# Kernel tuning notes

Hardware: AMD Instinct MI355X
Metric: run time of the kernel (lower is better)

## Reference

```python
import jax, jax.numpy as jnp
import numpy as np

B, N, D, H, COND = 1, 1024, 1024, 16, 128
S = 2 * N          # noisy tokens + clean x0 tokens
BS = 16            # diffusion block size
HD = D // H        # head dim = 64


def _ln(x, w):
    # LayerNorm module: F.layer_norm in fp32, then scale by weight (no bias)
    x = x.astype(jnp.float32)
    mu = jnp.mean(x, axis=-1, keepdims=True)
    var = jnp.var(x, axis=-1, keepdims=True)
    return (x - mu) / jnp.sqrt(var + 1e-5) * w


def _rotate_half(x):
    x1, x2 = jnp.split(x, 2, axis=-1)
    return jnp.concatenate([-x2, x1], axis=-1)


def _block_diff_mask(s, n, bs):
    q = jnp.arange(s)[:, None]
    k = jnp.arange(s)[None, :]
    fq = q >= n
    fk = k >= n
    bq = jnp.where(fq, (q - n) // bs, q // bs)
    bk = jnp.where(fk, (k - n) // bs, k // bs)
    diag = (bq == bk) & (fq == fk)
    off = (bq > bk) & fk & (~fq)
    caus = (bq >= bk) & fk & fq
    return diag | off | caus


def setup_inputs() -> dict:
    key = jax.random.key(0)
    ks = jax.random.split(key, 8)
    inv = 1.0 / (10000.0 ** (jnp.arange(0, HD, 2, dtype=jnp.float32) / HD))  # [32]
    t = jnp.arange(N, dtype=jnp.float32)[:, None] * inv[None, :]
    return {
        "x": jax.random.normal(ks[0], (B, S, D), jnp.float32),
        "c": jax.random.normal(ks[1], (B, COND), jnp.float32),
        "cos": jnp.cos(t),
        "sin": jnp.sin(t),
        "norm1_w": jnp.ones((D,), jnp.float32),
        "qkv_w": jax.random.normal(ks[2], (3 * D, D), jnp.float32) * (D ** -0.5),
        "attn_out_w": jax.random.normal(ks[3], (D, D), jnp.float32) * (D ** -0.5),
        "norm2_w": jnp.ones((D,), jnp.float32),
        "mlp_w1": jax.random.normal(ks[4], (4 * D, D), jnp.float32) * (D ** -0.5),
        "mlp_b1": jnp.zeros((4 * D,), jnp.float32),
        "mlp_w2": jax.random.normal(ks[5], (D, 4 * D), jnp.float32) * ((4 * D) ** -0.5),
        "mlp_b2": jnp.zeros((D,), jnp.float32),
        "adaLN_w": jax.random.normal(ks[6], (6 * D, COND), jnp.float32) * 0.02,
        "adaLN_b": jax.random.normal(ks[7], (6 * D,), jnp.float32) * 0.02,
    }


def reference(x, c, cos, sin, norm1_w, qkv_w, attn_out_w, norm2_w,
              mlp_w1, mlp_b1, mlp_w2, mlp_b2, adaLN_w, adaLN_b):
    # adaLN modulation: [B, 6D] -> six [B, 1, D] tensors
    mods = (c @ adaLN_w.T + adaLN_b)[:, None, :]
    sh_msa, sc_msa, g_msa, sh_mlp, sc_mlp, g_mlp = jnp.split(mods, 6, axis=-1)

    x_skip = x
    h = _ln(x, norm1_w) * (1 + sc_msa) + sh_msa  # modulate_fused

    # rotary tables broadcast to qkv rank 5 (torchscript path: applied to q, k AND v)
    cs = jnp.concatenate([cos, cos], axis=-1)[None, :, None, None, :]  # [1,N,1,1,HD]
    sn = jnp.concatenate([sin, sin], axis=-1)[None, :, None, None, :]

    def qkv_of(xh):  # xh: [B, N, D]
        qkv = (xh @ qkv_w.T).reshape(B, N, 3, H, HD)
        return qkv * cs + _rotate_half(qkv) * sn

    # halves processed separately (both use positions 0..N-1), then concatenated
    qkv = jnp.concatenate([qkv_of(h[:, :N]), qkv_of(h[:, N:])], axis=1)  # [B,S,3,H,HD]

    q = jnp.transpose(qkv[:, :, 0], (0, 2, 1, 3))  # [B,H,S,HD]
    k = jnp.transpose(qkv[:, :, 1], (0, 2, 1, 3))
    v = jnp.transpose(qkv[:, :, 2], (0, 2, 1, 3))

    scores = jnp.einsum('bhqd,bhkd->bhqk', q, k) / np.sqrt(HD).astype(np.float32)
    mask = _block_diff_mask(S, N, BS)  # [S,S] bool, block-diag | offset-causal | block-causal
    scores = jnp.where(mask[None, None], scores, -jnp.inf)
    attn = jax.nn.softmax(scores, axis=-1)
    o = jnp.einsum('bhqk,bhkd->bhqd', attn, v)
    o = jnp.transpose(o, (0, 2, 1, 3)).reshape(B, S, D)

    # inference bias_dropout_add_scale: gate * out + residual (dropout is identity)
    x2 = g_msa * (o @ attn_out_w.T) + x_skip
    h2 = _ln(x2, norm2_w) * (1 + sc_mlp) + sh_mlp
    m = jax.nn.gelu(h2 @ mlp_w1.T + mlp_b1, approximate=True) @ mlp_w2.T + mlp_b2
    return g_mlp * m + x2
```

## Files before the change

### kernel.cpp

```cpp
#include <hip/hip_runtime.h>
#include <math.h>

#define SS 2048
#define NN 1024
#define DD 1024
#define HH 16
#define CONDD 128

typedef unsigned short ushort;
typedef unsigned int uint;
typedef __bf16 bf16x8 __attribute__((ext_vector_type(8)));
typedef float f32x4 __attribute__((ext_vector_type(4)));
typedef short s16x4 __attribute__((ext_vector_type(4)));
typedef ushort u16x8 __attribute__((ext_vector_type(8)));

__device__ __forceinline__ float gelu_fast(float x) {
    float t = x + 0.044715f * x * x * x;
    float e = __builtin_exp2f(-2.3022081446f * t);
    return x * __builtin_amdgcn_rcpf(1.0f + e);
}

__device__ __forceinline__ ushort f2bf(float x) {
    uint u = __float_as_uint(x);
    u += 0x7fff + ((u >> 16) & 1);
    return (ushort)(u >> 16);
}

__device__ __forceinline__ float bf2f(ushort u) {
    return __uint_as_float(((uint)u) << 16);
}

__device__ __forceinline__ void gload16(const ushort* g, ushort* l) {
    __builtin_amdgcn_global_load_lds(
        (const __attribute__((address_space(1))) void*)g,
        (__attribute__((address_space(3))) void*)l, 16, 0, 0);
}

__device__ __forceinline__ f32x4 mfma16(s16x4 a, s16x4 b, f32x4 c) {
#if __has_builtin(__builtin_amdgcn_mfma_f32_16x16x16bf16_1k)
    return __builtin_amdgcn_mfma_f32_16x16x16bf16_1k(a, b, c, 0, 0, 0);
#else
    asm("v_mfma_f32_16x16x16_bf16 %0, %1, %2, %0" : "+v"(c) : "v"(a), "v"(b));
    return c;
#endif
}

__global__ void k_cast4(const float* __restrict__ s0, const float* __restrict__ s1,
                        const float* __restrict__ s2, const float* __restrict__ s3,
                        ushort* __restrict__ dst) {
    size_t gid = ((size_t)blockIdx.x * 256 + threadIdx.x) * 4;
    const float* src;
    size_t off;
    if (gid < (3ull << 20))      { src = s0; off = 0; }
    else if (gid < (4ull << 20)) { src = s1; off = 3ull << 20; }
    else if (gid < (8ull << 20)) { src = s2; off = 4ull << 20; }
    else                         { src = s3; off = 8ull << 20; }
    float4 v = *(const float4*)(src + (gid - off));
    ushort4 o = {f2bf(v.x), f2bf(v.y), f2bf(v.z), f2bf(v.w)};
    *(ushort4*)(dst + gid) = o;
}

__global__ void k_adaln(const float* __restrict__ c, const float* __restrict__ w,
                        const float* __restrict__ b, float* __restrict__ mods) {
    int o = blockIdx.x * 256 + threadIdx.x;
    float s = b[o];
    const float* wr = w + (size_t)o * CONDD;
    for (int k = 0; k < CONDD; ++k) s += c[k] * wr[k];
    mods[o] = s;
}

__global__ void k_ln_mod(const float* __restrict__ x, const float* __restrict__ w,
                         const float* __restrict__ mods, int sh_idx, int sc_idx,
                         ushort* __restrict__ out) {
    int row = blockIdx.x;
    int tid = threadIdx.x;
    const float* xr = x + (size_t)row * DD;
    float lx[4];
    float s = 0.f, s2 = 0.f;
    for (int i = 0; i < 4; ++i) {
        float v = xr[tid + i * 256];
        lx[i] = v; s += v; s2 += v * v;
    }
    __shared__ float rs[256], rs2[256];
    rs[tid] = s; rs2[tid] = s2; __syncthreads();
    for (int off = 128; off > 0; off >>= 1) {
        if (tid < off) { rs[tid] += rs[tid + off]; rs2[tid] += rs2[tid + off]; }
        __syncthreads();
    }
    float mu = rs[0] * (1.0f / DD);
    float var = rs2[0] * (1.0f / DD) - mu * mu;
    float rstd = rsqrtf(var + 1e-5f);
    const float* sh = mods + sh_idx * DD;
    const float* sc = mods + sc_idx * DD;
    ushort* orow = out + (size_t)row * DD;
    for (int i = 0; i < 4; ++i) {
        int d = tid + i * 256;
        orow[d] = f2bf((lx[i] - mu) * rstd * w[d] * (1.0f + sc[d]) + sh[d]);
    }
}

template <int TM, int MODE, typename OT>
__global__ void k_gemm_mfma(const ushort* __restrict__ A, const ushort* __restrict__ W,
                            const float* __restrict__ bias, const float* __restrict__ gate,
                            const float* __restrict__ resid, OT* __restrict__ C,
                            int M, int Nout, int K) {
    constexpr int WC = (TM == 128) ? 2 : 4;
    constexpr int MN = 128 / WC / 16;
    constexpr int BUFE = (TM + 128) * 64;
    __shared__ ushort lds[2 * BUFE];

    int tid = threadIdx.x;
    int lane = tid & 63, wave = tid >> 6;
    int wr = (TM == 128) ? (wave >> 1) : 0;
    int wc = (TM == 128) ? (wave & 1) : wave;
    int l15 = lane & 15, l4 = lane >> 4;

    int nwg = gridDim.x * gridDim.y;
    int orig = blockIdx.y * gridDim.x + blockIdx.x;
    int q = nwg >> 3, r = nwg & 7;
    int xcd = orig & 7, off = orig >> 3;
    int wgid = (xcd < r ? xcd * (q + 1) : r * (q + 1) + (xcd - r) * q) + off;
    int n0 = (wgid % gridDim.x) * 128;
    int m0 = (wgid / gridDim.x) * TM;

    f32x4 acc[4][MN] = {};

    auto stage = [&](int buf, int k0) {
        ushort* base = lds + buf * BUFE;
#pragma unroll
        for (int i = 0; i < TM / 32; ++i) {
            int cb = (wave * (TM / 32) + i) * 64;
            int ch = cb + lane;
            int row = ch >> 3;
            int kc = (ch & 7) ^ (row & 7);
            gload16(A + (size_t)(m0 + row) * K + k0 + kc * 8, base + cb * 8);
        }
#pragma unroll
        for (int i = 0; i < 4; ++i) {
            int cb = (wave * 4 + i) * 64;
            int ch = cb + lane;
            int row = ch >> 3;
            int kc = (ch & 7) ^ (row & 7);
            gload16(W + (size_t)(n0 + row) * K + k0 + kc * 8, base + TM * 64 + cb * 8);
        }
    };

    auto compute = [&](int buf) {
        const ushort* lA = lds + buf * BUFE;
        const ushort* lB = lA + TM * 64;
#pragma unroll
        for (int sub = 0; sub < 2; ++sub) {
            bf16x8 af[4], bw[MN];
#pragma unroll
            for (int mi = 0; mi < 4; ++mi) {
                int row = wr * 64 + mi * 16 + l15;
                int pos = ((sub << 2) | l4) ^ (row & 7);
                af[mi] = *(const bf16x8*)&lA[row * 64 + pos * 8];
            }
#pragma unroll
            for (int ni = 0; ni < MN; ++ni) {
                int row = wc * (MN * 16) + ni * 16 + l15;
                int pos = ((sub << 2) | l4) ^ (row & 7);
                bw[ni] = *(const bf16x8*)&lB[row * 64 + pos * 8];
            }
#pragma unroll
            for (int mi = 0; mi < 4; ++mi)
#pragma unroll
                for (int ni = 0; ni < MN; ++ni)
                    acc[mi][ni] = __builtin_amdgcn_mfma_f32_16x16x32_bf16(
                        af[mi], bw[ni], acc[mi][ni], 0, 0, 0);
        }
    };

    stage(0, 0);
    __syncthreads();
    int nk = K >> 6;
    for (int t = 0; t < nk; ++t) {
        if (t + 1 < nk) stage((t + 1) & 1, (t + 1) << 6);
        compute(t & 1);
        __syncthreads();
    }

#pragma unroll
    for (int mi = 0; mi < 4; ++mi) {
#pragma unroll
        for (int r2 = 0; r2 < 4; ++r2) {
            int m = m0 + wr * 64 + mi * 16 + l4 * 4 + r2;
#pragma unroll
            for (int ni = 0; ni < MN; ++ni) {
                int n = n0 + wc * (MN * 16) + ni * 16 + l15;
                float v = acc[mi][ni][r2];
                if (MODE == 1) v = gate[n] * v + resid[(size_t)m * Nout + n];
                if (MODE == 2) v = gelu_fast(v + bias[n]);
                if (MODE == 3) v = gate[n] * (v + bias[n]) + resid[(size_t)m * Nout + n];
                if (sizeof(OT) == 2) C[(size_t)m * Nout + n] = (OT)f2bf(v);
                else                 C[(size_t)m * Nout + n] = (OT)v;
            }
        }
    }
}

__global__ void k_rope2(const ushort* __restrict__ qkvb, const float* __restrict__ cosT,
                        const float* __restrict__ sinT, ushort* __restrict__ qb,
                        ushort* __restrict__ kb, ushort* __restrict__ vT) {
    __shared__ ushort vt[64][65];
    int h = blockIdx.x & 15;
    int st = blockIdx.x >> 4;
    int s0 = st * 64;
    int tid = threadIdx.x;
#pragma unroll
    for (int i = 0; i < 8; ++i) {
        int idx = tid + i * 256;
        int sl = idx >> 5, j = idx & 31;
        int s = s0 + sl;
        int pos = s & (NN - 1);
        float cv = cosT[pos * 32 + j], sv = sinT[pos * 32 + j];
        const ushort* row = qkvb + (size_t)s * 3072 + h * 64;
        float x1 = bf2f(row[j]), x2 = bf2f(row[j + 32]);
        qb[(size_t)s * DD + h * 64 + j]      = f2bf((x1 * cv - x2 * sv) * 0.18033688011f);
        qb[(size_t)s * DD + h * 64 + j + 32] = f2bf((x2 * cv + x1 * sv) * 0.18033688011f);
        x1 = bf2f(row[1024 + j]); x2 = bf2f(row[1024 + j + 32]);
        kb[(size_t)s * DD + h * 64 + j]      = f2bf(x1 * cv - x2 * sv);
        kb[(size_t)s * DD + h * 64 + j + 32] = f2bf(x2 * cv + x1 * sv);
        x1 = bf2f(row[2048 + j]); x2 = bf2f(row[2048 + j + 32]);
        vt[sl][j]      = f2bf(x1 * cv - x2 * sv);
        vt[sl][j + 32] = f2bf(x2 * cv + x1 * sv);
    }
    __syncthreads();
    int drow = tid >> 2, sc = (tid & 3) * 16;
    u16x8 a, b;
#pragma unroll
    for (int i = 0; i < 8; ++i) { a[i] = vt[sc + i][drow]; b[i] = vt[sc + 8 + i][drow]; }
    size_t base = (size_t)(h * 64 + drow) * SS + s0 + sc;
    *(u16x8*)&vT[base] = a;
    *(u16x8*)&vT[base + 8] = b;
}

struct KVTile { bf16x8 k0, k1; s16x4 v0, v1, v2, v3; };

__global__ __launch_bounds__(64) void k_attn3(
        const ushort* __restrict__ qb, const ushort* __restrict__ kb,
        const ushort* __restrict__ vT, ushort* __restrict__ o) {
    int id = blockIdx.x;
    int h = id & 15;
    int bq = 63 - (id >> 4);
    int lane = threadIdx.x;
    int l15 = lane & 15, l4 = lane >> 4;
    int hb = h * 64;

    const int q0A = bq * 16, q0B = NN + bq * 16;
    bf16x8 qA0 = *(const bf16x8*)&qb[(size_t)(q0A + l15) * DD + hb + l4 * 8];
    bf16x8 qA1 = *(const bf16x8*)&qb[(size_t)(q0A + l15) * DD + hb + 32 + l4 * 8];
    bf16x8 qB0 = *(const bf16x8*)&qb[(size_t)(q0B + l15) * DD + hb + l4 * 8];
    bf16x8 qB1 = *(const bf16x8*)&qb[(size_t)(q0B + l15) * DD + hb + 32 + l4 * 8];

    float mA = -1e30f, lA = 0.f, mB = -1e30f, lB = 0.f;
    f32x4 oA0 = {}, oA1 = {}, oA2 = {}, oA3 = {};
    f32x4 oB0 = {}, oB1 = {}, oB2 = {}, oB3 = {};

    auto loadT = [&](int kbase) {
        KVTile t;
        const ushort* kr = kb + (size_t)(kbase + l15) * DD + hb + l4 * 8;
        t.k0 = *(const bf16x8*)kr;
        t.k1 = *(const bf16x8*)(kr + 32);
        const ushort* vr = vT + (size_t)(hb + l15) * SS + kbase + l4 * 4;
        t.v0 = *(const s16x4*)vr;
        t.v1 = *(const s16x4*)(vr + 16 * SS);
        t.v2 = *(const s16x4*)(vr + 32 * SS);
        t.v3 = *(const s16x4*)(vr + 48 * SS);
        return t;
    };

    auto step = [&](const KVTile& t, bf16x8 Q0, bf16x8 Q1, float& m, float& l,
                    f32x4& O0, f32x4& O1, f32x4& O2, f32x4& O3) {
        f32x4 s = {};
        s = __builtin_amdgcn_mfma_f32_16x16x32_bf16(t.k0, Q0, s, 0, 0, 0);
        s = __builtin_amdgcn_mfma_f32_16x16x32_bf16(t.k1, Q1, s, 0, 0, 0);
        float tm = fmaxf(fmaxf(s[0], s[1]), fmaxf(s[2], s[3]));
        tm = fmaxf(tm, __shfl_xor(tm, 16));
        tm = fmaxf(tm, __shfl_xor(tm, 32));
        if (!__all(tm <= m + 8.0f)) {
            float mn = fmaxf(m, tm);
            float alpha = exp2f(m - mn);
            l *= alpha;
            O0 *= alpha; O1 *= alpha; O2 *= alpha; O3 *= alpha;
            m = mn;
        }
        float p0 = exp2f(s[0] - m), p1 = exp2f(s[1] - m);
        float p2 = exp2f(s[2] - m), p3 = exp2f(s[3] - m);
        float rsum = (p0 + p1) + (p2 + p3);
        rsum += __shfl_xor(rsum, 16);
        rsum += __shfl_xor(rsum, 32);
        l += rsum;
        s16x4 pf;
        pf[0] = (short)f2bf(p0); pf[1] = (short)f2bf(p1);
        pf[2] = (short)f2bf(p2); pf[3] = (short)f2bf(p3);
        O0 = mfma16(t.v0, pf, O0);
        O1 = mfma16(t.v1, pf, O1);
        O2 = mfma16(t.v2, pf, O2);
        O3 = mfma16(t.v3, pf, O3);
    };

    KVTile tA = loadT(bq * 16);
    KVTile tB = loadT(NN + bq * 16);
    KVTile cur, nxt;
    if (bq > 0) cur = loadT(NN);
    step(tA, qA0, qA1, mA, lA, oA0, oA1, oA2, oA3);
    step(tB, qB0, qB1, mB, lB, oB0, oB1, oB2, oB3);
    for (int t = 0; t < bq; ++t) {
        int tn = (t + 1 < bq) ? t + 1 : bq - 1;
        nxt = loadT(NN + tn * 16);
        step(cur, qA0, qA1, mA, lA, oA0, oA1, oA2, oA3);
        step(cur, qB0, qB1, mB, lB, oB0, oB1, oB2, oB3);
        cur = nxt;
    }

    float invA = 1.0f / lA, invB = 1.0f / lB;
    auto st4 = [&](ushort* p, f32x4 v) {
        ushort4 w = {f2bf(v[0]), f2bf(v[1]), f2bf(v[2]), f2bf(v[3])};
        *(ushort4*)p = w;
    };
    ushort* orA = o + (size_t)(q0A + l15) * DD + hb + l4 * 4;
    st4(orA,      oA0 * invA);
    st4(orA + 16, oA1 * invA);
    st4(orA + 32, oA2 * invA);
    st4(orA + 48, oA3 * invA);
    ushort* orB = o + (size_t)(q0B + l15) * DD + hb + l4 * 4;
    st4(orB,      oB0 * invB);
    st4(orB + 16, oB1 * invB);
    st4(orB + 32, oB2 * invB);
    st4(orB + 48, oB3 * invB);
}

extern "C" void kernel_launch(void* const* d_in, const int* in_sizes, int n_in,
                              void* d_out, int out_size, void* d_ws, size_t ws_size,
                              hipStream_t stream) {
    const float* x          = (const float*)d_in[0];
    const float* c          = (const float*)d_in[1];
    const float* cosT       = (const float*)d_in[2];
    const float* sinT       = (const float*)d_in[3];
    const float* norm1_w    = (const float*)d_in[4];
    const float* qkv_w      = (const float*)d_in[5];
    const float* attn_out_w = (const float*)d_in[6];
    const float* norm2_w    = (const float*)d_in[7];
    const float* mlp_w1     = (const float*)d_in[8];
    const float* mlp_b1     = (const float*)d_in[9];
    const float* mlp_w2     = (const float*)d_in[10];
    const float* mlp_b2     = (const float*)d_in[11];
    const float* adaLN_w    = (const float*)d_in[12];
    const float* adaLN_b    = (const float*)d_in[13];
    float* out = (float*)d_out;

    char* p = (char*)d_ws;
    float*  mods = (float*)p;   p += 6 * DD * 4;
    ushort* qkvb = (ushort*)p;  p += (size_t)SS * 3 * DD * 2;
    ushort* qb   = (ushort*)p;  p += (size_t)SS * DD * 2;
    ushort* kb   = (ushort*)p;  p += (size_t)SS * DD * 2;
    ushort* vT   = (ushort*)p;  p += (size_t)SS * DD * 2;
    float*  x2   = (float*)p;   p += (size_t)SS * DD * 4;
    ushort* hbuf = (ushort*)p;  p += (size_t)SS * DD * 2;
    ushort* obuf = (ushort*)p;  p += (size_t)SS * DD * 2;
    ushort* wq   = (ushort*)p;  p += (size_t)3 * DD * DD * 2;
    ushort* wo   = (ushort*)p;  p += (size_t)DD * DD * 2;
    ushort* w1   = (ushort*)p;  p += (size_t)4 * DD * DD * 2;
    ushort* w2   = (ushort*)p;  p += (size_t)4 * DD * DD * 2;
    ushort* m1   = qkvb;

    k_cast4<<<(12 << 20) / 1024, 256, 0, stream>>>(qkv_w, attn_out_w, mlp_w1, mlp_w2, wq);

    k_adaln<<<6 * DD / 256, 256, 0, stream>>>(c, adaLN_w, adaLN_b, mods);
    k_ln_mod<<<SS, 256, 0, stream>>>(x, norm1_w, mods, 0, 1, hbuf);

    dim3 g1(3 * DD / 128, SS / 64);
    k_gemm_mfma<64, 0, ushort><<<g1, 256, 0, stream>>>(hbuf, wq, nullptr, nullptr,
                                                       nullptr, qkvb, SS, 3 * DD, DD);
    k_rope2<<<512, 256, 0, stream>>>(qkvb, cosT, sinT, qb, kb, vT);
    k_attn3<<<HH * 64, 64, 0, stream>>>(qb, kb, vT, obuf);

    dim3 g2(DD / 128, SS / 64);
    k_gemm_mfma<64, 1, float><<<g2, 256, 0, stream>>>(obuf, wo, nullptr, mods + 2 * DD,
                                                      x, x2, SS, DD, DD);
    k_ln_mod<<<SS, 256, 0, stream>>>(x2, norm2_w, mods, 3, 4, hbuf);

    dim3 g3(4 * DD / 128, SS / 64);
    k_gemm_mfma<64, 2, ushort><<<g3, 256, 0, stream>>>(hbuf, w1, mlp_b1, nullptr,
                                                       nullptr, m1, SS, 4 * DD, DD);
    dim3 g4(DD / 128, SS / 64);
    k_gemm_mfma<64, 3, float><<<g4, 256, 0, stream>>>(m1, w2, mlp_b2, mods + 5 * DD,
                                                      x2, out, SS, DD, 4 * DD);
}
```

Measured before the change: 183.4 us.

## Split attention KV loop across four waves with LDS softmax merge

The attention kernel moves from one wave per block to four waves. Each wave handles every fourth KV tile with its own online-softmax state, and the partial max, sum and output are then combined through shared memory before a single vectorized store. This shortens the serial KV loop for the long causal rows, which should reduce tail latency and improve load balance across query blocks. The cost is extra LDS traffic, a block barrier and the merge arithmetic, and waves beyond bq sit idle for the short rows.

Result: faster. 169.7 us (-7.5%).

```diff
diff --git a/kernel.cpp b/kernel.cpp
--- a/kernel.cpp
+++ b/kernel.cpp
@@ -238,13 +238,18 @@
 
 struct KVTile { bf16x8 k0, k1; s16x4 v0, v1, v2, v3; };
 
-__global__ __launch_bounds__(64) void k_attn3(
+__global__ __launch_bounds__(256) void k_attn4(
         const ushort* __restrict__ qb, const ushort* __restrict__ kb,
         const ushort* __restrict__ vT, ushort* __restrict__ o) {
+    __shared__ float Ml[2][4][16], Ll[2][4][16];
+    __shared__ float Ob[2][4][16][68];
+
     int id = blockIdx.x;
     int h = id & 15;
     int bq = 63 - (id >> 4);
-    int lane = threadIdx.x;
+    int tid = threadIdx.x;
+    int wave = tid >> 6;
+    int lane = tid & 63;
     int l15 = lane & 15, l4 = lane >> 4;
     int hb = h * 64;
 
@@ -301,35 +306,52 @@
         O3 = mfma16(t.v3, pf, O3);
     };
 
-    KVTile tA = loadT(bq * 16);
-    KVTile tB = loadT(NN + bq * 16);
+    if (wave == 0) {
+        KVTile td = loadT(q0A);
+        step(td, qA0, qA1, mA, lA, oA0, oA1, oA2, oA3);
+    }
     KVTile cur, nxt;
-    if (bq > 0) cur = loadT(NN);
-    step(tA, qA0, qA1, mA, lA, oA0, oA1, oA2, oA3);
-    step(tB, qB0, qB1, mB, lB, oB0, oB1, oB2, oB3);
-    for (int t = 0; t < bq; ++t) {
-        int tn = (t + 1 < bq) ? t + 1 : bq - 1;
-        nxt = loadT(NN + tn * 16);
-        step(cur, qA0, qA1, mA, lA, oA0, oA1, oA2, oA3);
+    if (wave <= bq) cur = loadT(NN + wave * 16);
+    for (int t = wave; t <= bq; t += 4) {
+        int tn = t + 4;
+        if (tn <= bq) nxt = loadT(NN + tn * 16);
+        if (t < bq) step(cur, qA0, qA1, mA, lA, oA0, oA1, oA2, oA3);
         step(cur, qB0, qB1, mB, lB, oB0, oB1, oB2, oB3);
         cur = nxt;
     }
 
-    float invA = 1.0f / lA, invB = 1.0f / lB;
-    auto st4 = [&](ushort* p, f32x4 v) {
-        ushort4 w = {f2bf(v[0]), f2bf(v[1]), f2bf(v[2]), f2bf(v[3])};
-        *(ushort4*)p = w;
-    };
-    ushort* orA = o + (size_t)(q0A + l15) * DD + hb + l4 * 4;
-    st4(orA,      oA0 * invA);
-    st4(orA + 16, oA1 * invA);
-    st4(orA + 32, oA2 * invA);
-    st4(orA + 48, oA3 * invA);
-    ushort* orB = o + (size_t)(q0B + l15) * DD + hb + l4 * 4;
-    st4(orB,      oB0 * invB);
-    st4(orB + 16, oB1 * invB);
-    st4(orB + 32, oB2 * invB);
-    st4(orB + 48, oB3 * invB);
+    if (l4 == 0) {
+        Ml[0][wave][l15] = mA; Ll[0][wave][l15] = lA;
+        Ml[1][wave][l15] = mB; Ll[1][wave][l15] = lB;
+    }
+    *(f32x4*)&Ob[0][wave][l15][l4 * 4]      = oA0;
+    *(f32x4*)&Ob[0][wave][l15][l4 * 4 + 16] = oA1;
+    *(f32x4*)&Ob[0][wave][l15][l4 * 4 + 32] = oA2;
+    *(f32x4*)&Ob[0][wave][l15][l4 * 4 + 48] = oA3;
+    *(f32x4*)&Ob[1][wave][l15][l4 * 4]      = oB0;
+    *(f32x4*)&Ob[1][wave][l15][l4 * 4 + 16] = oB1;
+    *(f32x4*)&Ob[1][wave][l15][l4 * 4 + 32] = oB2;
+    *(f32x4*)&Ob[1][wave][l15][l4 * 4 + 48] = oB3;
+    __syncthreads();
+
+    int s = tid >> 7;
+    int qr = (tid >> 3) & 15;
+    int db = (tid & 7) * 8;
+    float m0 = Ml[s][0][qr], m1 = Ml[s][1][qr], m2 = Ml[s][2][qr], m3 = Ml[s][3][qr];
+    float ms = fmaxf(fmaxf(m0, m1), fmaxf(m2, m3));
+    float a0 = exp2f(m0 - ms), a1 = exp2f(m1 - ms);
+    float a2 = exp2f(m2 - ms), a3 = exp2f(m3 - ms);
+    float lt = a0 * Ll[s][0][qr] + a1 * Ll[s][1][qr] + a2 * Ll[s][2][qr] + a3 * Ll[s][3][qr];
+    float inv = 1.0f / lt;
+    int q0s = (s == 0) ? q0A : q0B;
+    u16x8 outv;
+#pragma unroll
+    for (int j = 0; j < 8; ++j) {
+        float v = a0 * Ob[s][0][qr][db + j] + a1 * Ob[s][1][qr][db + j] +
+                  a2 * Ob[s][2][qr][db + j] + a3 * Ob[s][3][qr][db + j];
+        outv[j] = f2bf(v * inv);
+    }
+    *(u16x8*)&o[(size_t)(q0s + qr) * DD + hb + db] = outv;
 }
 
 extern "C" void kernel_launch(void* const* d_in, const int* in_sizes, int n_in,
@@ -375,7 +397,7 @@
     k_gemm_mfma<64, 0, ushort><<<g1, 256, 0, stream>>>(hbuf, wq, nullptr, nullptr,
                                                        nullptr, qkvb, SS, 3 * DD, DD);
     k_rope2<<<512, 256, 0, stream>>>(qkvb, cosT, sinT, qb, kb, vT);
-    k_attn3<<<HH * 64, 64, 0, stream>>>(qb, kb, vT, obuf);
+    k_attn4<<<HH * 64, 256, 0, stream>>>(qb, kb, vT, obuf);
 
     dim3 g2(DD / 128, SS / 64);
     k_gemm_mfma<64, 1, float><<<g2, 256, 0, stream>>>(obuf, wo, nullptr, mods + 2 * DD,
```
